# Kernel tuning notes

Hardware: AMD Instinct MI355X
Metric: run time of the kernel (lower is better)

## Reference

```python
import jax, jax.numpy as jnp
import numpy as np

N = 100000
E = 3200000
F_IN, F_HID, F_OUT = 512, 16, 40


def setup_inputs() -> dict:
    key = jax.random.key(0)
    k1, k2, k3, k4 = jax.random.split(key, 4)
    x = jax.random.normal(k1, (N, F_IN), dtype=jnp.float32)
    edge_index = jax.random.randint(k2, (2, E), 0, N, dtype=jnp.int64)
    # Glorot-style init for the two GCN layer weights + zero biases
    W1 = jax.random.normal(k3, (F_IN, F_HID), dtype=jnp.float32) / np.sqrt(F_IN)
    b1 = jnp.zeros((F_HID,), dtype=jnp.float32)
    W2 = jax.random.normal(k4, (F_HID, F_OUT), dtype=jnp.float32) / np.sqrt(F_HID)
    b2 = jnp.zeros((F_OUT,), dtype=jnp.float32)
    return {"x": x, "edge_index": edge_index, "W1": W1, "b1": b1, "W2": W2, "b2": b2}


def _gcn_conv(x, src, dst, W, b):
    # x' = D^{-1/2} (A + I) D^{-1/2} (x W) + b   (standard GCNConv with self-loops)
    n = x.shape[0]
    h = x @ W  # [N, F_out] -- transform first (cheap edge traffic)
    deg = jax.ops.segment_sum(jnp.ones_like(dst, dtype=h.dtype), dst, num_segments=n) + 1.0  # +1 self-loop
    dinv = jax.lax.rsqrt(deg)
    msgs = h[src] * (dinv[src] * dinv[dst])[:, None]  # [E, F_out]
    agg = jax.ops.segment_sum(msgs, dst, num_segments=n)
    agg = agg + h * (dinv * dinv)[:, None]  # self-loop contribution
    return agg + b


def reference(x, edge_index, W1, b1, W2, b2):
    src, dst = edge_index[0], edge_index[1]
    h = _gcn_conv(x, src, dst, W1, b1)
    h = jax.nn.relu(h)
    # dropout is identity in eval mode (training=False)
    h = _gcn_conv(h, src, dst, W2, b2)
    return jax.nn.log_softmax(h, axis=1)
```

## Files before the change

### kernel.cpp

```cpp
#include <hip/hip_runtime.h>
#include <math.h>

#define FIN 512
#define FH 16
#define FOUT 40


__global__ void count_k(const int* __restrict__ dst, int E, int* __restrict__ cnt) {
  int e = blockIdx.x * blockDim.x + threadIdx.x;
  if (e < E) atomicAdd(&cnt[dst[e]], 1);
}

__global__ __launch_bounds__(1024) void scan_k(const int* __restrict__ cnt, int n,
                                               int* __restrict__ off, int* __restrict__ cur,
                                               float* __restrict__ dinv) {
  __shared__ int wsum[16];
  __shared__ int carry_s;
  const int tid = threadIdx.x;
  const int lane = tid & 63, wid = tid >> 6;
  if (tid == 0) carry_s = 0;
  __syncthreads();
  const int CH = 1024 * 8;
  const int nch = (n + CH - 1) / CH;
  for (int c = 0; c < nch; ++c) {
    int base = carry_s;
    int i0 = c * CH + tid * 8;
    int v[8], pre[8];
#pragma unroll
    for (int u = 0; u < 8; ++u) { int i = i0 + u; v[u] = (i < n) ? cnt[i] : 0; }
    int t = 0;
#pragma unroll
    for (int u = 0; u < 8; ++u) { pre[u] = t; t += v[u]; }
    int incl = t;
#pragma unroll
    for (int d = 1; d < 64; d <<= 1) {
      int o = __shfl_up(incl, d);
      if (lane >= d) incl += o;
    }
    if (lane == 63) wsum[wid] = incl;
    __syncthreads();
    int wexcl = 0;
#pragma unroll
    for (int w = 0; w < 16; ++w) if (w < wid) wexcl += wsum[w];
    int texcl = base + wexcl + (incl - t);
#pragma unroll
    for (int u = 0; u < 8; ++u) {
      int i = i0 + u;
      if (i < n) {
        int o = texcl + pre[u];
        off[i] = o; cur[i] = o;
        dinv[i] = rsqrtf((float)v[u] + 1.0f);
      }
    }
    __syncthreads();
    if (tid == 1023) carry_s = base + wexcl + incl;
    __syncthreads();
  }
  if (tid == 0) off[n] = carry_s;
}

__global__ void scatter_k(const int* __restrict__ src, const int* __restrict__ dst, int E,
                          int* __restrict__ cur, int* __restrict__ ssrc) {
  int e = blockIdx.x * blockDim.x + threadIdx.x;
  if (e < E) {
    int p = atomicAdd(&cur[dst[e]], 1);
    ssrc[p] = src[e];
  }
}


__global__ __launch_bounds__(256) void gemm1_k(const float* __restrict__ x,
                                               const float* __restrict__ W1,
                                               const float* __restrict__ dinv, int n,
                                               float* __restrict__ hs1) {
  __shared__ float w1s[FIN * FH];
  for (int idx = threadIdx.x; idx < FIN * FH; idx += 256) w1s[idx] = W1[idx];
  __syncthreads();

  const int row_raw = blockIdx.x * 256 + threadIdx.x;
  const int row = row_raw < n ? row_raw : n - 1;
  const float4* __restrict__ xr = (const float4*)(x + (size_t)row * FIN);

  float4 a0 = {0, 0, 0, 0}, a1 = {0, 0, 0, 0}, a2 = {0, 0, 0, 0}, a3 = {0, 0, 0, 0};

#pragma unroll 2
  for (int it = 0; it < FIN / 4; ++it) {
    float4 xv = xr[it];
    const float* wf = w1s + it * 4 * FH;
#pragma unroll
    for (int j = 0; j < 4; ++j) {
      const float xj = (j == 0) ? xv.x : (j == 1) ? xv.y : (j == 2) ? xv.z : xv.w;
      const float* wj = wf + j * FH;
      float4 w0 = *(const float4*)(wj + 0);
      float4 w1 = *(const float4*)(wj + 4);
      float4 w2 = *(const float4*)(wj + 8);
      float4 w3 = *(const float4*)(wj + 12);
      a0.x += xj * w0.x; a0.y += xj * w0.y; a0.z += xj * w0.z; a0.w += xj * w0.w;
      a1.x += xj * w1.x; a1.y += xj * w1.y; a1.z += xj * w1.z; a1.w += xj * w1.w;
      a2.x += xj * w2.x; a2.y += xj * w2.y; a2.z += xj * w2.z; a2.w += xj * w2.w;
      a3.x += xj * w3.x; a3.y += xj * w3.y; a3.z += xj * w3.z; a3.w += xj * w3.w;
    }
  }

  if (row_raw < n) {
    const float di = dinv[row];
    float4* o = (float4*)(hs1 + (size_t)row * FH);
    a0.x *= di; a0.y *= di; a0.z *= di; a0.w *= di;
    a1.x *= di; a1.y *= di; a1.z *= di; a1.w *= di;
    a2.x *= di; a2.y *= di; a2.z *= di; a2.w *= di;
    a3.x *= di; a3.y *= di; a3.z *= di; a3.w *= di;
    o[0] = a0; o[1] = a1; o[2] = a2; o[3] = a3;
  }
}


__global__ __launch_bounds__(256) void gather1_k(const float* __restrict__ hs1,
                                                 const int* __restrict__ off,
                                                 const int* __restrict__ ssrc,
                                                 const float* __restrict__ dinv,
                                                 const float* __restrict__ b1, int n,
                                                 float* __restrict__ rs) {
  const int lane = threadIdx.x & 63;
  const int wid = threadIdx.x >> 6;
  const int i = blockIdx.x * 4 + wid;
  if (i >= n) return;
  const int k = lane & 15, esub = lane >> 4;
  const int jb = off[i], je = off[i + 1];
  float acc = 0.f;
  int j = jb + esub;
  int s = (j < je) ? ssrc[j] : -1;
  while (s >= 0) {
    const int j2 = j + 4;
    const int s2 = (j2 < je) ? ssrc[j2] : -1;
    acc += hs1[(size_t)s * FH + k];
    j = j2; s = s2;
  }
  if (esub == 0) acc += hs1[(size_t)i * FH + k];
  acc += __shfl_xor(acc, 16);
  acc += __shfl_xor(acc, 32);
  if (lane < 16) {
    const float di = dinv[i];
    float v = di * acc + b1[k];
    rs[(size_t)i * FH + k] = (v > 0.f ? v : 0.f) * di;
  }
}


__global__ __launch_bounds__(256) void gather2_k(const float* __restrict__ rs,
                                                 const int* __restrict__ off,
                                                 const int* __restrict__ ssrc,
                                                 const float* __restrict__ dinv,
                                                 const float* __restrict__ W2,
                                                 const float* __restrict__ b2, int n,
                                                 float* __restrict__ out) {
  __shared__ float w2s[FH * FOUT + FOUT];
  for (int idx = threadIdx.x; idx < FH * FOUT + FOUT; idx += 256)
    w2s[idx] = (idx < FH * FOUT) ? W2[idx] : b2[idx - FH * FOUT];
  __syncthreads();

  const int lane = threadIdx.x & 63;
  const int wid = threadIdx.x >> 6;
  const int i = blockIdx.x * 4 + wid;
  if (i >= n) return;
  const int k = lane & 15, esub = lane >> 4;
  const int jb = off[i], je = off[i + 1];
  float acc = 0.f;
  int j = jb + esub;
  int s = (j < je) ? ssrc[j] : -1;
  while (s >= 0) {
    const int j2 = j + 4;
    const int s2 = (j2 < je) ? ssrc[j2] : -1;
    acc += rs[(size_t)s * FH + k];
    j = j2; s = s2;
  }
  if (esub == 0) acc += rs[(size_t)i * FH + k];
  acc += __shfl_xor(acc, 16);
  acc += __shfl_xor(acc, 32);
  acc *= dinv[i];

  float hv = (lane < FOUT) ? w2s[FH * FOUT + lane] : 0.f;
#pragma unroll
  for (int kk = 0; kk < 16; ++kk) {
    const float a = __shfl(acc, kk);
    if (lane < FOUT) hv += a * w2s[kk * FOUT + lane];
  }

  float m = (lane < FOUT) ? hv : -INFINITY;
#pragma unroll
  for (int d = 1; d < 64; d <<= 1) m = fmaxf(m, __shfl_xor(m, d));
  float ex = (lane < FOUT) ? expf(hv - m) : 0.f;
#pragma unroll
  for (int d = 1; d < 64; d <<= 1) ex += __shfl_xor(ex, d);
  if (lane < FOUT) out[(size_t)i * FOUT + lane] = hv - m - logf(ex);
}


extern "C" void kernel_launch(void* const* d_in, const int* in_sizes, int n_in,
                              void* d_out, int out_size, void* d_ws, size_t ws_size,
                              hipStream_t stream) {
  const float* x  = (const float*)d_in[0];
  const int*   ei = (const int*)d_in[1];
  const float* W1 = (const float*)d_in[2];
  const float* b1 = (const float*)d_in[3];
  const float* W2 = (const float*)d_in[4];
  const float* b2 = (const float*)d_in[5];
  float* out = (float*)d_out;

  const int n = in_sizes[0] / FIN;
  const int E = in_sizes[1] / 2;
  const int* src = ei;
  const int* dst = ei + E;

  char* ws = (char*)d_ws;
  size_t o = 0;
  auto alloc = [&](size_t bytes) {
    void* p = ws + o;
    o = (o + bytes + 255) & ~(size_t)255;
    return p;
  };
  int*   cnt  = (int*)alloc((size_t)n * 4);
  int*   off  = (int*)alloc((size_t)(n + 1) * 4);
  int*   cur  = (int*)alloc((size_t)n * 4);
  float* dinv = (float*)alloc((size_t)n * 4);
  int*   ssrc = (int*)alloc((size_t)E * 4);
  float* hs1  = (float*)alloc((size_t)n * FH * 4);
  float* rsb  = (float*)alloc((size_t)n * FH * 4);

  hipMemsetAsync(cnt, 0, (size_t)n * 4, stream);

  int egrid = (E + 255) / 256;
  count_k<<<egrid, 256, 0, stream>>>(dst, E, cnt);
  scan_k<<<1, 1024, 0, stream>>>(cnt, n, off, cur, dinv);
  scatter_k<<<egrid, 256, 0, stream>>>(src, dst, E, cur, ssrc);

  gemm1_k<<<(n + 255) / 256, 256, 0, stream>>>(x, W1, dinv, n, hs1);
  gather1_k<<<(n + 3) / 4, 256, 0, stream>>>(hs1, off, ssrc, dinv, b1, n, rsb);
  gather2_k<<<(n + 3) / 4, 256, 0, stream>>>(rsb, off, ssrc, dinv, W2, b2, n, out);
}
```

Baseline: 805.0 us.

## Replace per-node CSR build with coarse bucket binning and shared-memory aggregation

Result: slower. 883.7 us (+9.8%).

```diff
diff --git a/kernel.cpp b/kernel.cpp
--- a/kernel.cpp
+++ b/kernel.cpp
@@ -4,70 +4,134 @@
 #define FIN 512
 #define FH 16
 #define FOUT 40
-
-
-__global__ void count_k(const int* __restrict__ dst, int E, int* __restrict__ cnt) {
-  int e = blockIdx.x * blockDim.x + threadIdx.x;
-  if (e < E) atomicAdd(&cnt[dst[e]], 1);
-}
-
-__global__ __launch_bounds__(1024) void scan_k(const int* __restrict__ cnt, int n,
-                                               int* __restrict__ off, int* __restrict__ cur,
-                                               float* __restrict__ dinv) {
-  __shared__ int wsum[16];
-  __shared__ int carry_s;
-  const int tid = threadIdx.x;
-  const int lane = tid & 63, wid = tid >> 6;
-  if (tid == 0) carry_s = 0;
-  __syncthreads();
-  const int CH = 1024 * 8;
-  const int nch = (n + CH - 1) / CH;
-  for (int c = 0; c < nch; ++c) {
-    int base = carry_s;
-    int i0 = c * CH + tid * 8;
-    int v[8], pre[8];
-#pragma unroll
-    for (int u = 0; u < 8; ++u) { int i = i0 + u; v[u] = (i < n) ? cnt[i] : 0; }
-    int t = 0;
-#pragma unroll
-    for (int u = 0; u < 8; ++u) { pre[u] = t; t += v[u]; }
-    int incl = t;
-#pragma unroll
-    for (int d = 1; d < 64; d <<= 1) {
-      int o = __shfl_up(incl, d);
-      if (lane >= d) incl += o;
-    }
-    if (lane == 63) wsum[wid] = incl;
-    __syncthreads();
-    int wexcl = 0;
-#pragma unroll
-    for (int w = 0; w < 16; ++w) if (w < wid) wexcl += wsum[w];
-    int texcl = base + wexcl + (incl - t);
-#pragma unroll
-    for (int u = 0; u < 8; ++u) {
-      int i = i0 + u;
-      if (i < n) {
-        int o = texcl + pre[u];
-        off[i] = o; cur[i] = o;
-        dinv[i] = rsqrtf((float)v[u] + 1.0f);
-      }
-    }
-    __syncthreads();
-    if (tid == 1023) carry_s = base + wexcl + incl;
-    __syncthreads();
-  }
-  if (tid == 0) off[n] = carry_s;
-}
-
-__global__ void scatter_k(const int* __restrict__ src, const int* __restrict__ dst, int E,
-                          int* __restrict__ cur, int* __restrict__ ssrc) {
-  int e = blockIdx.x * blockDim.x + threadIdx.x;
-  if (e < E) {
-    int p = atomicAdd(&cur[dst[e]], 1);
-    ssrc[p] = src[e];
-  }
-}
-
+#define RANGE 128
+#define RSH 7
+#define NB_MAX 1024
+#define SRC_BITS 17
+#define SRC_MASK 0x1FFFF
+#define BCHUNK 4096
+#define HCHUNK 16384
+
+__global__ __launch_bounds__(256) void histA_k(const int* __restrict__ dst, int E, int NB,
+                                               unsigned* __restrict__ bcnt) {
+  __shared__ unsigned h[NB_MAX];
+  for (int b = threadIdx.x; b < NB; b += 256) h[b] = 0;
+  __syncthreads();
+  const int base = blockIdx.x * HCHUNK;
+  const int cn = min(HCHUNK, E - base);
+  for (int u = threadIdx.x; u < cn; u += 256)
+    atomicAdd(&h[((unsigned)dst[base + u]) >> RSH], 1u);
+  __syncthreads();
+  for (int b = threadIdx.x; b < NB; b += 256) {
+    unsigned c = h[b];
+    if (c) atomicAdd(&bcnt[b], c);
+  }
+}
+
+__global__ __launch_bounds__(1024) void scanB_k(const unsigned* __restrict__ bcnt, int NB,
+                                                unsigned* __restrict__ boff,
+                                                unsigned* __restrict__ bcur) {
+  __shared__ unsigned ws[16];
+  const int t = threadIdx.x, lane = t & 63, wid = t >> 6;
+  unsigned v = (t < NB) ? bcnt[t] : 0;
+  unsigned incl = v;
+#pragma unroll
+  for (int d = 1; d < 64; d <<= 1) {
+    unsigned o = __shfl_up(incl, d);
+    if (lane >= d) incl += o;
+  }
+  if (lane == 63) ws[wid] = incl;
+  __syncthreads();
+  unsigned woff = 0, tot = 0;
+#pragma unroll
+  for (int w = 0; w < 16; ++w) {
+    unsigned s = ws[w];
+    if (w < wid) woff += s;
+    tot += s;
+  }
+  unsigned ex = woff + incl - v;
+  if (t < NB) { boff[t] = ex; bcur[t] = ex; }
+  if (t == 0) boff[NB] = tot;
+}
+
+__global__ __launch_bounds__(256) void bin_k(const int* __restrict__ src,
+                                             const int* __restrict__ dst, int E, int NB,
+                                             unsigned* __restrict__ bcur,
+                                             unsigned* __restrict__ bins) {
+  __shared__ unsigned hist[NB_MAX];
+  __shared__ unsigned excl[NB_MAX];
+  __shared__ unsigned gbase[NB_MAX];
+  __shared__ unsigned lcur[NB_MAX];
+  __shared__ unsigned stage[BCHUNK];
+  __shared__ unsigned short sbkt[BCHUNK];
+  __shared__ unsigned wtot[4];
+  const int t = threadIdx.x, lane = t & 63, wid = t >> 6;
+  for (int b = t; b < NB; b += 256) hist[b] = 0;
+  __syncthreads();
+  const int base = blockIdx.x * BCHUNK;
+  const int cn = min(BCHUNK, E - base);
+  for (int u = t; u < cn; u += 256)
+    atomicAdd(&hist[((unsigned)dst[base + u]) >> RSH], 1u);
+  __syncthreads();
+  unsigned loc[4], s = 0;
+#pragma unroll
+  for (int j = 0; j < 4; ++j) {
+    int idx = t * 4 + j;
+    loc[j] = s;
+    s += (idx < NB) ? hist[idx] : 0;
+  }
+  unsigned incl = s;
+#pragma unroll
+  for (int d = 1; d < 64; d <<= 1) {
+    unsigned o = __shfl_up(incl, d);
+    if (lane >= d) incl += o;
+  }
+  if (lane == 63) wtot[wid] = incl;
+  __syncthreads();
+  unsigned woff = 0;
+  for (int w = 0; w < wid; ++w) woff += wtot[w];
+  unsigned tex = woff + incl - s;
+#pragma unroll
+  for (int j = 0; j < 4; ++j) {
+    int idx = t * 4 + j;
+    if (idx < NB) excl[idx] = tex + loc[j];
+  }
+  __syncthreads();
+  for (int b = t; b < NB; b += 256) {
+    unsigned c = hist[b];
+    gbase[b] = c ? atomicAdd(&bcur[b], c) : 0u;
+    lcur[b] = excl[b];
+  }
+  __syncthreads();
+  for (int u = t; u < cn; u += 256) {
+    int e = base + u;
+    unsigned d = (unsigned)dst[e];
+    unsigned bkt = d >> RSH;
+    unsigned pk = ((unsigned)src[e]) | ((d & (RANGE - 1)) << SRC_BITS);
+    unsigned lr = atomicAdd(&lcur[bkt], 1u);
+    stage[lr] = pk;
+    sbkt[lr] = (unsigned short)bkt;
+  }
+  __syncthreads();
+  for (int u = t; u < cn; u += 256) {
+    unsigned bkt = sbkt[u];
+    bins[gbase[bkt] + (u - excl[bkt])] = stage[u];
+  }
+}
+
+__global__ __launch_bounds__(256) void deg_k(const unsigned* __restrict__ boff,
+                                             const unsigned* __restrict__ bins, int n,
+                                             float* __restrict__ dinv) {
+  __shared__ unsigned dh[RANGE];
+  const int t = threadIdx.x, b = blockIdx.x;
+  if (t < RANGE) dh[t] = 0;
+  __syncthreads();
+  const unsigned jb = boff[b], je = boff[b + 1];
+  for (unsigned j = jb + t; j < je; j += 256) atomicAdd(&dh[bins[j] >> SRC_BITS], 1u);
+  __syncthreads();
+  const int i = b * RANGE + t;
+  if (t < RANGE && i < n) dinv[i] = rsqrtf((float)dh[t] + 1.0f);
+}
 
 __global__ __launch_bounds__(256) void gemm1_k(const float* __restrict__ x,
                                                const float* __restrict__ W1,
@@ -113,87 +177,113 @@
   }
 }
 
-
 __global__ __launch_bounds__(256) void gather1_k(const float* __restrict__ hs1,
-                                                 const int* __restrict__ off,
-                                                 const int* __restrict__ ssrc,
+                                                 const unsigned* __restrict__ boff,
+                                                 const unsigned* __restrict__ bins,
                                                  const float* __restrict__ dinv,
                                                  const float* __restrict__ b1, int n,
                                                  float* __restrict__ rs) {
-  const int lane = threadIdx.x & 63;
-  const int wid = threadIdx.x >> 6;
-  const int i = blockIdx.x * 4 + wid;
-  if (i >= n) return;
-  const int k = lane & 15, esub = lane >> 4;
-  const int jb = off[i], je = off[i + 1];
-  float acc = 0.f;
-  int j = jb + esub;
-  int s = (j < je) ? ssrc[j] : -1;
-  while (s >= 0) {
-    const int j2 = j + 4;
-    const int s2 = (j2 < je) ? ssrc[j2] : -1;
-    acc += hs1[(size_t)s * FH + k];
-    j = j2; s = s2;
-  }
-  if (esub == 0) acc += hs1[(size_t)i * FH + k];
-  acc += __shfl_xor(acc, 16);
-  acc += __shfl_xor(acc, 32);
-  if (lane < 16) {
-    const float di = dinv[i];
-    float v = di * acc + b1[k];
-    rs[(size_t)i * FH + k] = (v > 0.f ? v : 0.f) * di;
-  }
-}
-
+  __shared__ float acc[RANGE * FH];
+  __shared__ float b1s[FH];
+  const int t = threadIdx.x, b = blockIdx.x;
+  if (t < FH) b1s[t] = b1[t];
+  for (int u = t; u < RANGE * FH; u += 256) acc[u] = 0.f;
+  __syncthreads();
+  const unsigned jb = boff[b], je = boff[b + 1];
+  const int k = t & 15, slot = t >> 4;
+  for (unsigned j = jb + slot; j < je; j += 16) {
+    const unsigned pv = bins[j];
+    const int s = pv & SRC_MASK;
+    const int dl = pv >> SRC_BITS;
+    atomicAdd(&acc[dl * FH + k], hs1[(size_t)s * FH + k]);
+  }
+  __syncthreads();
+  const int base = b * RANGE;
+  const float4* acc4 = (const float4*)acc;
+#pragma unroll
+  for (int q = 0; q < 2; ++q) {
+    const int fi = t + q * 256;
+    const int node = fi >> 2, sub = fi & 3;
+    const int i = base + node;
+    if (i < n) {
+      float4 a = acc4[fi];
+      float4 hv = ((const float4*)hs1)[(size_t)i * 4 + sub];
+      const float d = dinv[i];
+      float4 r;
+      r.x = (a.x + hv.x) * d + b1s[sub * 4 + 0];
+      r.y = (a.y + hv.y) * d + b1s[sub * 4 + 1];
+      r.z = (a.z + hv.z) * d + b1s[sub * 4 + 2];
+      r.w = (a.w + hv.w) * d + b1s[sub * 4 + 3];
+      r.x = (r.x > 0.f ? r.x : 0.f) * d;
+      r.y = (r.y > 0.f ? r.y : 0.f) * d;
+      r.z = (r.z > 0.f ? r.z : 0.f) * d;
+      r.w = (r.w > 0.f ? r.w : 0.f) * d;
+      ((float4*)rs)[(size_t)i * 4 + sub] = r;
+    }
+  }
+}
 
 __global__ __launch_bounds__(256) void gather2_k(const float* __restrict__ rs,
-                                                 const int* __restrict__ off,
-                                                 const int* __restrict__ ssrc,
+                                                 const unsigned* __restrict__ boff,
+                                                 const unsigned* __restrict__ bins,
                                                  const float* __restrict__ dinv,
                                                  const float* __restrict__ W2,
                                                  const float* __restrict__ b2, int n,
                                                  float* __restrict__ out) {
+  __shared__ float acc[RANGE * FH];
   __shared__ float w2s[FH * FOUT + FOUT];
-  for (int idx = threadIdx.x; idx < FH * FOUT + FOUT; idx += 256)
+  const int t = threadIdx.x, b = blockIdx.x;
+  for (int idx = t; idx < FH * FOUT + FOUT; idx += 256)
     w2s[idx] = (idx < FH * FOUT) ? W2[idx] : b2[idx - FH * FOUT];
-  __syncthreads();
-
-  const int lane = threadIdx.x & 63;
-  const int wid = threadIdx.x >> 6;
-  const int i = blockIdx.x * 4 + wid;
-  if (i >= n) return;
-  const int k = lane & 15, esub = lane >> 4;
-  const int jb = off[i], je = off[i + 1];
-  float acc = 0.f;
-  int j = jb + esub;
-  int s = (j < je) ? ssrc[j] : -1;
-  while (s >= 0) {
-    const int j2 = j + 4;
-    const int s2 = (j2 < je) ? ssrc[j2] : -1;
-    acc += rs[(size_t)s * FH + k];
-    j = j2; s = s2;
-  }
-  if (esub == 0) acc += rs[(size_t)i * FH + k];
-  acc += __shfl_xor(acc, 16);
-  acc += __shfl_xor(acc, 32);
-  acc *= dinv[i];
-
-  float hv = (lane < FOUT) ? w2s[FH * FOUT + lane] : 0.f;
-#pragma unroll
-  for (int kk = 0; kk < 16; ++kk) {
-    const float a = __shfl(acc, kk);
-    if (lane < FOUT) hv += a * w2s[kk * FOUT + lane];
-  }
-
-  float m = (lane < FOUT) ? hv : -INFINITY;
-#pragma unroll
-  for (int d = 1; d < 64; d <<= 1) m = fmaxf(m, __shfl_xor(m, d));
-  float ex = (lane < FOUT) ? expf(hv - m) : 0.f;
-#pragma unroll
-  for (int d = 1; d < 64; d <<= 1) ex += __shfl_xor(ex, d);
-  if (lane < FOUT) out[(size_t)i * FOUT + lane] = hv - m - logf(ex);
-}
-
+  for (int u = t; u < RANGE * FH; u += 256) acc[u] = 0.f;
+  __syncthreads();
+  const unsigned jb = boff[b], je = boff[b + 1];
+  const int k = t & 15, slot = t >> 4;
+  for (unsigned j = jb + slot; j < je; j += 16) {
+    const unsigned pv = bins[j];
+    const int s = pv & SRC_MASK;
+    const int dl = pv >> SRC_BITS;
+    atomicAdd(&acc[dl * FH + k], rs[(size_t)s * FH + k]);
+  }
+  __syncthreads();
+  const int base = b * RANGE;
+  float4* acc4 = (float4*)acc;
+#pragma unroll
+  for (int q = 0; q < 2; ++q) {
+    const int fi = t + q * 256;
+    const int node = fi >> 2, sub = fi & 3;
+    const int i = base + node;
+    if (i < n) {
+      float4 a = acc4[fi];
+      float4 r = ((const float4*)rs)[(size_t)i * 4 + sub];
+      const float d = dinv[i];
+      a.x = (a.x + r.x) * d;
+      a.y = (a.y + r.y) * d;
+      a.z = (a.z + r.z) * d;
+      a.w = (a.w + r.w) * d;
+      acc4[fi] = a;
+    }
+  }
+  __syncthreads();
+  const int lane = t & 63, wv = t >> 6;
+  for (int nd = wv; nd < RANGE; nd += 4) {
+    const int i = base + nd;
+    if (i >= n) continue;
+    float hv = (lane < FOUT) ? w2s[FH * FOUT + lane] : 0.f;
+#pragma unroll
+    for (int kk = 0; kk < 16; ++kk) {
+      const float a = acc[nd * FH + kk];
+      if (lane < FOUT) hv += a * w2s[kk * FOUT + lane];
+    }
+    float m = (lane < FOUT) ? hv : -INFINITY;
+#pragma unroll
+    for (int d = 1; d < 64; d <<= 1) m = fmaxf(m, __shfl_xor(m, d));
+    float ex = (lane < FOUT) ? expf(hv - m) : 0.f;
+#pragma unroll
+    for (int d = 1; d < 64; d <<= 1) ex += __shfl_xor(ex, d);
+    if (lane < FOUT) out[(size_t)i * FOUT + lane] = hv - m - logf(ex);
+  }
+}
 
 extern "C" void kernel_launch(void* const* d_in, const int* in_sizes, int n_in,
                               void* d_out, int out_size, void* d_ws, size_t ws_size,
@@ -210,6 +300,7 @@
   const int E = in_sizes[1] / 2;
   const int* src = ei;
   const int* dst = ei + E;
+  const int NB = (n + RANGE - 1) >> RSH;
 
   char* ws = (char*)d_ws;
   size_t o = 0;
@@ -218,22 +309,22 @@
     o = (o + bytes + 255) & ~(size_t)255;
     return p;
   };
-  int*   cnt  = (int*)alloc((size_t)n * 4);
-  int*   off  = (int*)alloc((size_t)(n + 1) * 4);
-  int*   cur  = (int*)alloc((size_t)n * 4);
-  float* dinv = (float*)alloc((size_t)n * 4);
-  int*   ssrc = (int*)alloc((size_t)E * 4);
-  float* hs1  = (float*)alloc((size_t)n * FH * 4);
-  float* rsb  = (float*)alloc((size_t)n * FH * 4);
-
-  hipMemsetAsync(cnt, 0, (size_t)n * 4, stream);
-
-  int egrid = (E + 255) / 256;
-  count_k<<<egrid, 256, 0, stream>>>(dst, E, cnt);
-  scan_k<<<1, 1024, 0, stream>>>(cnt, n, off, cur, dinv);
-  scatter_k<<<egrid, 256, 0, stream>>>(src, dst, E, cur, ssrc);
+  unsigned* bcnt = (unsigned*)alloc((size_t)(NB + 1) * 4);
+  unsigned* boff = (unsigned*)alloc((size_t)(NB + 1) * 4);
+  unsigned* bcur = (unsigned*)alloc((size_t)NB * 4);
+  float*    dinv = (float*)alloc((size_t)n * 4);
+  unsigned* bins = (unsigned*)alloc((size_t)E * 4);
+  float*    hs1  = (float*)alloc((size_t)n * FH * 4);
+  float*    rsb  = (float*)alloc((size_t)n * FH * 4);
+
+  hipMemsetAsync(bcnt, 0, (size_t)(NB + 1) * 4, stream);
+
+  histA_k<<<(E + HCHUNK - 1) / HCHUNK, 256, 0, stream>>>(dst, E, NB, bcnt);
+  scanB_k<<<1, 1024, 0, stream>>>(bcnt, NB, boff, bcur);
+  bin_k<<<(E + BCHUNK - 1) / BCHUNK, 256, 0, stream>>>(src, dst, E, NB, bcur, bins);
+  deg_k<<<NB, 256, 0, stream>>>(boff, bins, n, dinv);
 
   gemm1_k<<<(n + 255) / 256, 256, 0, stream>>>(x, W1, dinv, n, hs1);
-  gather1_k<<<(n + 3) / 4, 256, 0, stream>>>(hs1, off, ssrc, dinv, b1, n, rsb);
-  gather2_k<<<(n + 3) / 4, 256, 0, stream>>>(rsb, off, ssrc, dinv, W2, b2, n, out);
-}
+  gather1_k<<<NB, 256, 0, stream>>>(hs1, boff, bins, dinv, b1, n, rsb);
+  gather2_k<<<NB, 256, 0, stream>>>(rsb, boff, bins, dinv, W2, b2, n, out);
+}
```
